# Kernel tuning notes

Measured on AMD Instinct MI355X. Metric: run time of the kernel, lower is better.

Reference implementation:

```python
import jax, jax.numpy as jnp
import numpy as np

D = 512
H = 8
FFN_H = 2048
NEG = -1.0e10


def layer_norm(x, gamma, beta, eps=1e-5):
    mu = jnp.mean(x, axis=-1, keepdims=True)
    var = jnp.var(x, axis=-1, keepdims=True)
    return (x - mu) * jax.lax.rsqrt(var + eps) * gamma + beta


def mha(x_q, x_kv, Wq, Wk, Wv, Wo, valid_lens):
    # x_q: [B,Tq,D], x_kv: [B,Tk,D]; valid_lens: [B,Tq] or [B]
    B, Tq, _ = x_q.shape
    Tk = x_kv.shape[1]
    dh = D // H
    q = (x_q @ Wq.T).reshape(B, Tq, H, dh).transpose(0, 2, 1, 3)  # [B,H,Tq,dh]
    k = (x_kv @ Wk.T).reshape(B, Tk, H, dh).transpose(0, 2, 1, 3)
    v = (x_kv @ Wv.T).reshape(B, Tk, H, dh).transpose(0, 2, 1, 3)
    scores = jnp.einsum('bhqd,bhkd->bhqk', q, k) / jnp.sqrt(jnp.float32(dh))
    pos = jnp.arange(Tk)
    if valid_lens.ndim == 1:  # [B] -> mask [B,1,1,Tk]
        mask = pos[None, None, None, :] < valid_lens[:, None, None, None]
    else:  # [B,Tq] -> mask [B,1,Tq,Tk]
        mask = pos[None, None, None, :] < valid_lens[:, None, :, None]
    scores = jnp.where(mask, scores, NEG)
    attn = jax.nn.softmax(scores, axis=-1)
    out = jnp.einsum('bhqk,bhkd->bhqd', attn, v)  # [B,H,Tq,dh]
    out = out.transpose(0, 2, 1, 3).reshape(B, Tq, D)
    return out @ Wo.T


def setup_inputs() -> dict:
    key = jax.random.key(0)
    ks = jax.random.split(key, 20)
    B, T = 32, 512
    s = 1.0 / np.sqrt(D)
    inp = {
        'X': jax.random.normal(ks[0], (B, T, D), jnp.float32),
        'enc_outputs': jax.random.normal(ks[1], (B, T, D), jnp.float32),
        'dec_valid_lens': jax.random.randint(ks[2], (B, T), 1, T + 1, jnp.int32),
        'enc_valid_lens': jax.random.randint(ks[3], (B,), 1, T + 1, jnp.int32),
    }
    names = ['Wq1', 'Wk1', 'Wv1', 'Wo1', 'Wq2', 'Wk2', 'Wv2', 'Wo2']
    for i, n in enumerate(names):
        inp[n] = jax.random.normal(ks[4 + i], (D, D), jnp.float32) * s
    inp['W1'] = jax.random.normal(ks[12], (FFN_H, D), jnp.float32) * s
    inp['b1'] = jnp.zeros((FFN_H,), jnp.float32)
    inp['W2'] = jax.random.normal(ks[13], (D, FFN_H), jnp.float32) * (1.0 / np.sqrt(FFN_H))
    inp['b2'] = jnp.zeros((D,), jnp.float32)
    for j in (1, 2, 3):
        inp[f'g{j}'] = jnp.ones((D,), jnp.float32)
        inp[f'be{j}'] = jnp.zeros((D,), jnp.float32)
    return inp


def reference(X, enc_outputs, dec_valid_lens, enc_valid_lens,
              Wq1, Wk1, Wv1, Wo1, Wq2, Wk2, Wv2, Wo2,
              W1, b1, W2, b2, g1, be1, g2, be2, g3, be3):
    # Training path: state[2][i] is None -> key_values = X. Dropout in eval mode (identity).
    X2 = mha(X, X, Wq1, Wk1, Wv1, Wo1, dec_valid_lens)            # self-attention
    Y = layer_norm(X + X2, g1, be1)                               # AddNorm1
    Y2 = mha(Y, enc_outputs, Wq2, Wk2, Wv2, Wo2, enc_valid_lens)  # cross-attention
    Z = layer_norm(Y + Y2, g2, be2)                               # AddNorm2
    F = (jax.nn.leaky_relu(Z @ W1.T + b1, 0.01)) @ W2.T + b2      # FFN (LeakyReLU slope 0.01)
    return layer_norm(Z + F, g3, be3)                             # AddNorm3
```

## Files before the change

### kernel.cpp

```cpp
#include <hip/hip_runtime.h>
#include <cstdint>
#include <cstddef>

typedef __bf16 bf16;
typedef __bf16 bf16x8 __attribute__((ext_vector_type(8)));
typedef float  f32x4  __attribute__((ext_vector_type(4)));
typedef unsigned short u16;

#define MD ((size_t)8388608)

__device__ __forceinline__ void async_copy16(const bf16* gp, bf16* lp) {
  __builtin_amdgcn_global_load_lds(
      (__attribute__((address_space(1))) void*)(gp),
      (__attribute__((address_space(3))) void*)(lp), 16, 0, 0);
}

__device__ __forceinline__ int is_f32(const u16* __restrict__ x) {
  const int e = (x[(threadIdx.x & 63) * 2] >> 7) & 0xFF;
  return __ballot(e >= 141) != 0ull;
}

struct ConvSrc { const void* p[20]; };

__global__ __launch_bounds__(256)
void convert_all(ConvSrc s, bf16* __restrict__ ws, const u16* __restrict__ xprobe)
{
  const int n[20] = {8388608, 8388608,
                     262144, 262144, 262144, 262144, 262144, 262144, 262144, 262144,
                     1048576, 2048, 1048576, 512, 512, 512, 512, 512, 512, 512};
  const unsigned int doff[20] = {
      41943040u, 50331648u,
      58720256u, 58982400u, 59244544u, 59506688u,
      59768832u, 60030976u, 60293120u, 60555264u,
      60817408u, 61865984u, 61868032u, 62916608u,
      62917120u, 62917632u, 62918144u, 62918656u, 62919168u, 62919680u};

  const int f32 = is_f32(xprobe);

  int bi = blockIdx.x;
  int idx = 0, b0 = 0;
  for (; idx < 20; ++idx) {
    const int nb = (n[idx] + 2047) >> 11;
    if (bi < b0 + nb) break;
    b0 += nb;
  }
  const int i = ((bi - b0) << 11) + threadIdx.x * 8;
  if (i >= n[idx]) return;
  bf16* dst = ws + doff[idx] + i;
  if (f32) {
    const float* sp = (const float*)s.p[idx] + i;
    f32x4 a = *(const f32x4*)sp;
    f32x4 b = *(const f32x4*)(sp + 4);
    bf16x8 o;
#pragma unroll
    for (int e = 0; e < 4; ++e) { o[e] = (bf16)a[e]; o[4 + e] = (bf16)b[e]; }
    *(bf16x8*)dst = o;
  } else {
    *(bf16x8*)dst = *(const bf16x8*)((const bf16*)s.p[idx] + i);
  }
}

template<int MODE, int TM, int TN>
__global__ __launch_bounds__(256)
void gemm_bt(const bf16* __restrict__ A, const bf16* __restrict__ B,
             const bf16* __restrict__ bias, bf16* __restrict__ C,
             int M, int N, int K)
{
  constexpr int MI = TM / 32;
  constexpr int NJ = TN / 32;
  __shared__ __attribute__((aligned(16))) bf16 As[TM * 64];
  __shared__ __attribute__((aligned(16))) bf16 Bs[TN * 64];

  const int t    = threadIdx.x;
  const int wave = t >> 6;
  const int lane = t & 63;
  const int quad = lane >> 4;
  const int l15  = lane & 15;
  const int wr   = (wave >> 1) * (TM / 2);
  const int wc   = (wave & 1) * (TN / 2);

  const int id    = blockIdx.y * gridDim.x + blockIdx.x;
  const int chunk = (gridDim.x * gridDim.y) >> 3;
  const int lin   = (id & 7) * chunk + (id >> 3);
  const int m0    = (lin / gridDim.x) * TM;
  const int n0    = (lin % gridDim.x) * TN;

  const f32x4 fz = {0.f, 0.f, 0.f, 0.f};
  f32x4 acc[MI][NJ];
#pragma unroll
  for (int i = 0; i < MI; ++i)
#pragma unroll
    for (int j = 0; j < NJ; ++j) acc[i][j] = fz;

  const int nkt = K >> 6;
  for (int kt = 0; kt < nkt; ++kt) {
    const int k0 = kt << 6;
    __syncthreads();
#pragma unroll
    for (int c = 0; c < TM / 32; ++c) {
      const int s   = c * 256 + t;
      const int row = s >> 3;
      const int kg  = ((s & 7) ^ (row & 7)) << 3;
      async_copy16(A + (size_t)(m0 + row) * K + k0 + kg,
                   As + ((c * 256 + wave * 64) << 3));
    }
#pragma unroll
    for (int c = 0; c < TN / 32; ++c) {
      const int s   = c * 256 + t;
      const int row = s >> 3;
      const int kg  = ((s & 7) ^ (row & 7)) << 3;
      async_copy16(B + (size_t)(n0 + row) * K + k0 + kg,
                   Bs + ((c * 256 + wave * 64) << 3));
    }
    __syncthreads();

#pragma unroll
    for (int ks = 0; ks < 2; ++ks) {
      bf16x8 af[MI], bfv[NJ];
#pragma unroll
      for (int i = 0; i < MI; ++i) {
        const int row = wr + i * 16 + l15;
        const int ph  = (ks * 4 + quad) ^ (row & 7);
        af[i] = *(const bf16x8*)(As + row * 64 + ph * 8);
      }
#pragma unroll
      for (int j = 0; j < NJ; ++j) {
        const int row = wc + j * 16 + l15;
        const int ph  = (ks * 4 + quad) ^ (row & 7);
        bfv[j] = *(const bf16x8*)(Bs + row * 64 + ph * 8);
      }
#pragma unroll
      for (int i = 0; i < MI; ++i)
#pragma unroll
        for (int j = 0; j < NJ; ++j)
          acc[i][j] = __builtin_amdgcn_mfma_f32_16x16x32_bf16(af[i], bfv[j],
                                                              acc[i][j], 0, 0, 0);
    }
  }

#pragma unroll
  for (int i = 0; i < MI; ++i) {
    const int m = m0 + wr + i * 16 + quad * 4;
#pragma unroll
    for (int j = 0; j < NJ; ++j) {
      const int n = n0 + wc + j * 16 + l15;
      float bv = 0.f;
      if (MODE >= 1) bv = (float)bias[n];
#pragma unroll
      for (int r = 0; r < 4; ++r) {
        float v = acc[i][j][r];
        if (MODE >= 1) v += bv;
        if (MODE == 1) v = v > 0.f ? v : 0.01f * v;
        C[(size_t)(m + r) * N + n] = (bf16)v;
      }
    }
  }
}

template<int MODE, int BM>
__global__ __launch_bounds__(512, 1)
void gemm4p(const bf16* __restrict__ A, const bf16* __restrict__ B,
            const bf16* __restrict__ bias, bf16* __restrict__ C,
            int M, int N, int K)
{
  constexpr int BN = 256, T = 512, WM = 2, WN = 4;
  constexpr int WR = BM / WM;
  constexpr int MI = WR / 16;
  constexpr int NJ = 4;
  constexpr int MH = MI / 2;
  constexpr int LA = BM * 8 / T;
  constexpr int LB = 4;
  static_assert(LA == 4 || LA == 2, "schedule assumes BM in {256,128}");

  __shared__ __attribute__((aligned(16))) bf16 As[2][BM * 64];
  __shared__ __attribute__((aligned(16))) bf16 Bs[2][BN * 64];

  const int t    = threadIdx.x;
  const int lane = t & 63;
  const int quad = lane >> 4;
  const int l15  = lane & 15;
  const int wave = t >> 6;
  const int wm   = wave >> 2;
  const int wn   = wave & 3;

  const int id    = blockIdx.y * gridDim.x + blockIdx.x;
  const int chunk = (gridDim.x * gridDim.y) >> 3;
  const int lin   = (id & 7) * chunk + (id >> 3);
  const int m0    = (lin / gridDim.x) * BM;
  const int n0    = (lin % gridDim.x) * BN;

  const bf16* Ag = A + (size_t)m0 * K;
  const bf16* Bg = B + (size_t)n0 * K;
  const int wbase = wave << 6;

  auto stA = [&](int kt, int r, int buf) {
    const int s   = r * T + t;
    const int row = s >> 3;
    const int cg  = s & 7;
    async_copy16(Ag + (size_t)row * K + (kt << 6) + ((cg ^ (row & 7)) << 3),
                 &As[buf][(size_t)(r * T + wbase) << 3]);
  };
  auto stB = [&](int kt, int r, int buf) {
    const int s   = r * T + t;
    const int row = s >> 3;
    const int cg  = s & 7;
    async_copy16(Bg + (size_t)row * K + (kt << 6) + ((cg ^ (row & 7)) << 3),
                 &Bs[buf][(size_t)(r * T + wbase) << 3]);
  };
  auto ldfrag = [&](const bf16* base, int row, int ks) -> bf16x8 {
    return *(const bf16x8*)(base + row * 64 + ((((ks << 2) + quad) ^ (row & 7)) << 3));
  };

  const f32x4 fz = {0.f, 0.f, 0.f, 0.f};
  f32x4 acc[MI][NJ];
#pragma unroll
  for (int i = 0; i < MI; ++i)
#pragma unroll
    for (int j = 0; j < NJ; ++j) acc[i][j] = fz;

  const int nkt = K >> 6;

#pragma unroll
  for (int r = 0; r < LA; ++r) stA(0, r, 0);
#pragma unroll
  for (int r = 0; r < LB; ++r) stB(0, r, 0);
  if constexpr (LA == 4) { stA(1, 0, 1); stA(1, 2, 1); }
#pragma unroll
  for (int r = 0; r < LB; ++r) stB(1, r, 1);
  if constexpr (LA == 4) asm volatile("s_waitcnt vmcnt(6)" ::: "memory");
  else                   asm volatile("s_waitcnt vmcnt(4)" ::: "memory");
  __builtin_amdgcn_s_barrier();

  for (int j = 0; j < nkt; ++j) {
    const int cb = j & 1;
    const bf16* a_l = As[cb];
    const bf16* b_l = Bs[cb];
    const int kN = (j + 1 < nkt) ? j + 1 : nkt - 1;
    const int kF = (j + 2 < nkt) ? j + 2 : nkt - 1;

    bf16x8 bfv[NJ];
    bf16x8 af[MH];

#pragma unroll
    for (int nj = 0; nj < NJ; ++nj) bfv[nj] = ldfrag(b_l, wn * 64 + nj * 16 + l15, 0);
#pragma unroll
    for (int mi = 0; mi < MH; ++mi) af[mi] = ldfrag(a_l, wm * WR + mi * 16 + l15, 0);
    if constexpr (LA == 4) { stA(kN, 1, cb ^ 1); stA(kN, 3, cb ^ 1); }
    else                   { stA(kN, 0, cb ^ 1); stA(kN, 1, cb ^ 1); }
    __builtin_amdgcn_s_barrier();
    asm volatile("s_waitcnt lgkmcnt(0)" ::: "memory");
    __builtin_amdgcn_sched_barrier(0);
    __builtin_amdgcn_s_setprio(1);
#pragma unroll
    for (int mi = 0; mi < MH; ++mi)
#pragma unroll
      for (int nj = 0; nj < NJ; ++nj)
        acc[mi][nj] = __builtin_amdgcn_mfma_f32_16x16x32_bf16(af[mi], bfv[nj],
                                                              acc[mi][nj], 0, 0, 0);
    __builtin_amdgcn_s_setprio(0);
    __builtin_amdgcn_s_barrier();

#pragma unroll
    for (int mi = 0; mi < MH; ++mi) af[mi] = ldfrag(a_l, wm * WR + (MH + mi) * 16 + l15, 0);
    __builtin_amdgcn_s_barrier();
    asm volatile("s_waitcnt lgkmcnt(0)" ::: "memory");
    __builtin_amdgcn_sched_barrier(0);
    __builtin_amdgcn_s_setprio(1);
#pragma unroll
    for (int mi = 0; mi < MH; ++mi)
#pragma unroll
      for (int nj = 0; nj < NJ; ++nj)
        acc[MH + mi][nj] = __builtin_amdgcn_mfma_f32_16x16x32_bf16(af[mi], bfv[nj],
                                                                   acc[MH + mi][nj], 0, 0, 0);
    __builtin_amdgcn_s_setprio(0);
    __builtin_amdgcn_s_barrier();

#pragma unroll
    for (int nj = 0; nj < NJ; ++nj) bfv[nj] = ldfrag(b_l, wn * 64 + nj * 16 + l15, 1);
#pragma unroll
    for (int mi = 0; mi < MH; ++mi) af[mi] = ldfrag(a_l, wm * WR + mi * 16 + l15, 1);
    __builtin_amdgcn_s_barrier();
    asm volatile("s_waitcnt lgkmcnt(0)" ::: "memory");
    __builtin_amdgcn_sched_barrier(0);
    __builtin_amdgcn_s_setprio(1);
#pragma unroll
    for (int mi = 0; mi < MH; ++mi)
#pragma unroll
      for (int nj = 0; nj < NJ; ++nj)
        acc[mi][nj] = __builtin_amdgcn_mfma_f32_16x16x32_bf16(af[mi], bfv[nj],
                                                              acc[mi][nj], 0, 0, 0);
    __builtin_amdgcn_s_setprio(0);
    __builtin_amdgcn_s_barrier();

#pragma unroll
    for (int mi = 0; mi < MH; ++mi) af[mi] = ldfrag(a_l, wm * WR + (MH + mi) * 16 + l15, 1);
    if constexpr (LA == 4) { stA(kF, 0, cb); stA(kF, 2, cb); }
#pragma unroll
    for (int r = 0; r < LB; ++r) stB(kF, r, cb);
    __builtin_amdgcn_s_barrier();
    asm volatile("s_waitcnt lgkmcnt(0)" ::: "memory");
    __builtin_amdgcn_sched_barrier(0);
    __builtin_amdgcn_s_setprio(1);
#pragma unroll
    for (int mi = 0; mi < MH; ++mi)
#pragma unroll
      for (int nj = 0; nj < NJ; ++nj)
        acc[MH + mi][nj] = __builtin_amdgcn_mfma_f32_16x16x32_bf16(af[mi], bfv[nj],
                                                                   acc[MH + mi][nj], 0, 0, 0);
    __builtin_amdgcn_s_setprio(0);
    if constexpr (LA == 4) asm volatile("s_waitcnt vmcnt(6)" ::: "memory");
    else                   asm volatile("s_waitcnt vmcnt(4)" ::: "memory");
    __builtin_amdgcn_s_barrier();
  }

  asm volatile("s_waitcnt vmcnt(0)" ::: "memory");

#pragma unroll
  for (int mi = 0; mi < MI; ++mi) {
    const int m = m0 + wm * WR + mi * 16 + quad * 4;
#pragma unroll
    for (int nj = 0; nj < NJ; ++nj) {
      const int n = n0 + wn * 64 + nj * 16 + l15;
      float bv = 0.f;
      if (MODE >= 1) bv = (float)bias[n];
#pragma unroll
      for (int r = 0; r < 4; ++r) {
        float v = acc[mi][nj][r];
        if (MODE >= 1) v += bv;
        if (MODE == 1) v = v > 0.f ? v : 0.01f * v;
        C[(size_t)(m + r) * N + n] = (bf16)v;
      }
    }
  }
}

__global__ __launch_bounds__(256, 4)
void flash_attn(const bf16* __restrict__ Qp, const bf16* __restrict__ Kp,
                const bf16* __restrict__ Vp, bf16* __restrict__ Op,
                const int* __restrict__ vlen, int per_query, int sq, int skv)
{
  __shared__ __attribute__((aligned(16))) bf16 Ks[64][72];
  __shared__ __attribute__((aligned(16))) bf16 VsT[64][72];
  __shared__ __attribute__((aligned(16))) bf16 Ps[4][32][72];
  __shared__ int vlmax_sh;

  const int t    = threadIdx.x;
  const int wave = t >> 6;
  const int lane = t & 63;
  const int quad = lane >> 4;
  const int l15  = lane & 15;
  const int bx   = blockIdx.x;
  const int qt   = bx >> 8;
  const int h    = bx & 7;
  const int b    = (bx >> 3) & 31;
  const int q0   = qt * 128 + wave * 32;

  bf16x8 qfrag[2][2];
#pragma unroll
  for (int mt = 0; mt < 2; ++mt)
#pragma unroll
    for (int ks = 0; ks < 2; ++ks)
      qfrag[mt][ks] = *(const bf16x8*)(Qp +
          (size_t)(b * 512 + q0 + mt * 16 + l15) * sq + h * 64 + ks * 32 + quad * 8);

  int vl_r[2][4];
  int myvl = 1;
#pragma unroll
  for (int mt = 0; mt < 2; ++mt)
#pragma unroll
    for (int r = 0; r < 4; ++r) {
      const int q = q0 + mt * 16 + quad * 4 + r;
      const int v = per_query ? vlen[b * 512 + q] : vlen[b];
      vl_r[mt][r] = v;
      myvl = v > myvl ? v : myvl;
    }

  if (t == 0) vlmax_sh = 1;
  __syncthreads();
#pragma unroll
  for (int off = 1; off < 64; off <<= 1) {
    const int o = __shfl_xor(myvl, off);
    myvl = o > myvl ? o : myvl;
  }
  if (lane == 0) atomicMax(&vlmax_sh, myvl);
  __syncthreads();
  const int ktiles = (vlmax_sh + 63) >> 6;

  const f32x4 fz = {0.f, 0.f, 0.f, 0.f};
  float l_part[2][4] = {{0.f,0.f,0.f,0.f},{0.f,0.f,0.f,0.f}};
  f32x4 o_acc[2][4];
#pragma unroll
  for (int mt = 0; mt < 2; ++mt)
#pragma unroll
    for (int nt = 0; nt < 4; ++nt) o_acc[mt][nt] = fz;

  for (int kt = 0; kt < ktiles; ++kt) {
    const int k0 = kt * 64;
    __syncthreads();
    {
      const int r0 = t >> 3;
      const int c0 = (t & 7) * 8;
      const bf16* g = Kp + (size_t)(b * 512 + k0 + r0) * skv + h * 64 + c0;
      *(bf16x8*)&Ks[r0][c0]      = *(const bf16x8*)g;
      *(bf16x8*)&Ks[r0 + 32][c0] = *(const bf16x8*)(g + (size_t)32 * skv);
    }
    {
      const bf16* g = Vp + (size_t)(b * 512 + k0 + wave * 16) * skv + h * 64 + lane;
      bf16x8 lo, hi;
#pragma unroll
      for (int kk = 0; kk < 8; ++kk) lo[kk] = g[(size_t)kk * skv];
#pragma unroll
      for (int kk = 0; kk < 8; ++kk) hi[kk] = g[(size_t)(kk + 8) * skv];
      *(bf16x8*)&VsT[lane][wave * 16]     = lo;
      *(bf16x8*)&VsT[lane][wave * 16 + 8] = hi;
    }
    __syncthreads();

    f32x4 s[2][4];
#pragma unroll
    for (int mt = 0; mt < 2; ++mt)
#pragma unroll
      for (int nt = 0; nt < 4; ++nt) s[mt][nt] = fz;
#pragma unroll
    for (int ks = 0; ks < 2; ++ks)
#pragma unroll
      for (int nt = 0; nt < 4; ++nt) {
        const bf16x8 bk = *(const bf16x8*)&Ks[nt * 16 + l15][ks * 32 + quad * 8];
        s[0][nt] = __builtin_amdgcn_mfma_f32_16x16x32_bf16(qfrag[0][ks], bk, s[0][nt], 0, 0, 0);
        s[1][nt] = __builtin_amdgcn_mfma_f32_16x16x32_bf16(qfrag[1][ks], bk, s[1][nt], 0, 0, 0);
      }

#pragma unroll
    for (int mt = 0; mt < 2; ++mt)
#pragma unroll
      for (int nt = 0; nt < 4; ++nt) {
        const int k_abs = k0 + nt * 16 + l15;
#pragma unroll
        for (int r = 0; r < 4; ++r) {
          const float p = (k_abs < vl_r[mt][r]) ? __expf(s[mt][nt][r] * 0.125f) : 0.f;
          l_part[mt][r] += p;
          Ps[wave][mt * 16 + quad * 4 + r][nt * 16 + l15] = (bf16)p;
        }
      }

#pragma unroll
    for (int ks = 0; ks < 2; ++ks) {
      const bf16x8 ap0 = *(const bf16x8*)&Ps[wave][l15][ks * 32 + quad * 8];
      const bf16x8 ap1 = *(const bf16x8*)&Ps[wave][16 + l15][ks * 32 + quad * 8];
#pragma unroll
      for (int nt = 0; nt < 4; ++nt) {
        const bf16x8 bv = *(const bf16x8*)&VsT[nt * 16 + l15][ks * 32 + quad * 8];
        o_acc[0][nt] = __builtin_amdgcn_mfma_f32_16x16x32_bf16(ap0, bv, o_acc[0][nt], 0, 0, 0);
        o_acc[1][nt] = __builtin_amdgcn_mfma_f32_16x16x32_bf16(ap1, bv, o_acc[1][nt], 0, 0, 0);
      }
    }
  }

#pragma unroll
  for (int mt = 0; mt < 2; ++mt)
#pragma unroll
    for (int r = 0; r < 4; ++r) {
      float l = l_part[mt][r];
#pragma unroll
      for (int off = 1; off < 16; off <<= 1)
        l += __shfl_xor(l, off);
      const float inv_l = (l > 0.f) ? (1.f / l) : 0.f;
      const int q = q0 + mt * 16 + quad * 4 + r;
#pragma unroll
      for (int nt = 0; nt < 4; ++nt)
        Op[(size_t)(b * 512 + q) * 512 + h * 64 + nt * 16 + l15] =
            (bf16)(o_acc[mt][nt][r] * inv_l);
    }
}

__global__ __launch_bounds__(256)
void add_layernorm(const bf16* X, const bf16* R,
                   const bf16* __restrict__ gamma, const bf16* __restrict__ beta,
                   bf16* Out)
{
  const int t    = threadIdx.x;
  const int wave = t >> 6;
  const int lane = t & 63;
  const size_t row  = (size_t)blockIdx.x * 4 + wave;
  const size_t base = row * 512 + lane * 8;

  bf16x8 xv = *(const bf16x8*)(X + base);
  bf16x8 rv = *(const bf16x8*)(R + base);
  float v[8];
  float sum = 0.f, ss = 0.f;
#pragma unroll
  for (int i = 0; i < 8; ++i) {
    v[i] = (float)xv[i] + (float)rv[i];
    sum += v[i];
    ss  += v[i] * v[i];
  }
#pragma unroll
  for (int off = 1; off < 64; off <<= 1) {
    sum += __shfl_xor(sum, off);
    ss  += __shfl_xor(ss, off);
  }
  const float mean = sum * (1.f / 512.f);
  const float var  = ss * (1.f / 512.f) - mean * mean;
  const float rstd = rsqrtf(var + 1e-5f);

  bf16x8 gv = *(const bf16x8*)(gamma + lane * 8);
  bf16x8 bv = *(const bf16x8*)(beta + lane * 8);
  bf16x8 ov;
#pragma unroll
  for (int i = 0; i < 8; ++i)
    ov[i] = (bf16)(((v[i] - mean) * rstd) * (float)gv[i] + (float)bv[i]);
  *(bf16x8*)(Out + base) = ov;
}

__global__ __launch_bounds__(256)
void add_layernorm_out(const bf16* X, const bf16* R,
                       const bf16* __restrict__ gamma, const bf16* __restrict__ beta,
                       void* Out, const u16* __restrict__ xprobe)
{
  const int t    = threadIdx.x;
  const int wave = t >> 6;
  const int lane = t & 63;
  const size_t row  = (size_t)blockIdx.x * 4 + wave;
  const size_t base = row * 512 + lane * 8;

  const int f32 = is_f32(xprobe);

  bf16x8 xv = *(const bf16x8*)(X + base);
  bf16x8 rv = *(const bf16x8*)(R + base);
  float v[8];
  float sum = 0.f, ss = 0.f;
#pragma unroll
  for (int i = 0; i < 8; ++i) {
    v[i] = (float)xv[i] + (float)rv[i];
    sum += v[i];
    ss  += v[i] * v[i];
  }
#pragma unroll
  for (int off = 1; off < 64; off <<= 1) {
    sum += __shfl_xor(sum, off);
    ss  += __shfl_xor(ss, off);
  }
  const float mean = sum * (1.f / 512.f);
  const float var  = ss * (1.f / 512.f) - mean * mean;
  const float rstd = rsqrtf(var + 1e-5f);

  bf16x8 gv = *(const bf16x8*)(gamma + lane * 8);
  bf16x8 bv = *(const bf16x8*)(beta + lane * 8);
  float o[8];
#pragma unroll
  for (int i = 0; i < 8; ++i)
    o[i] = ((v[i] - mean) * rstd) * (float)gv[i] + (float)bv[i];

  if (f32) {
    float* op = (float*)Out + base;
    f32x4 o0 = {o[0], o[1], o[2], o[3]};
    f32x4 o1 = {o[4], o[5], o[6], o[7]};
    *(f32x4*)op       = o0;
    *(f32x4*)(op + 4) = o1;
  } else {
    bf16x8 ov;
#pragma unroll
    for (int i = 0; i < 8; ++i) ov[i] = (bf16)o[i];
    *(bf16x8*)((bf16*)Out + base) = ov;
  }
}

extern "C" void kernel_launch(void* const* d_in, const int* in_sizes, int n_in,
                              void* d_out, int out_size, void* d_ws, size_t ws_size,
                              hipStream_t stream)
{
  (void)in_sizes; (void)n_in; (void)out_size; (void)ws_size;

  const int* dvl = (const int*)d_in[2];
  const int* evl = (const int*)d_in[3];
  const u16* xprobe = (const u16*)d_in[0];

  bf16* ws = (bf16*)d_ws;
  bf16* S0 = ws;
  bf16* S1 = ws + 1 * MD;
  bf16* S3 = ws + 3 * MD;
  bf16* S4 = ws + 4 * MD;
  bf16* Xb = ws + 5 * MD;
  bf16* Eb = ws + 6 * MD;
  bf16* W  = ws + 7 * MD;
  const bf16 *Wq1 = W,
             *Wo1 = W + 786432,   *Wq2 = W + 1048576, *Wk2 = W + 1310720,
             *Wo2 = W + 1835008,
             *W1  = W + 2097152,  *b1  = W + 3145728,
             *W2  = W + 3147776,  *b2  = W + 4196352,
             *g1  = W + 4196864,  *be1 = W + 4197376,
             *g2  = W + 4197888,  *be2 = W + 4198400,
             *g3  = W + 4198912,  *be3 = W + 4199424;

  ConvSrc cs;
  cs.p[0] = d_in[0];  cs.p[1] = d_in[1];
  for (int k = 0; k < 12; ++k) cs.p[2 + k] = d_in[4 + k];
  for (int k = 0; k < 6; ++k)  cs.p[14 + k] = d_in[16 + k];
  convert_all<<<dim3(10248), dim3(256), 0, stream>>>(cs, ws, xprobe);

  dim3 blk256(256);
  dim3 blk512(512);
  dim3 gP(4, 128);

  gemm4p<0,256><<<dim3(6, 64), blk512, 0, stream>>>(Xb, Wq1, nullptr, S0, 16384, 1536, 512);
  flash_attn<<<dim3(1024), blk256, 0, stream>>>(S0, S0 + 512, S0 + 1024, S3, dvl, 1, 1536, 1536);
  gemm_bt<0,128,128><<<gP, blk256, 0, stream>>>(S3, Wo1, nullptr, S1, 16384, 512, 512);
  add_layernorm<<<dim3(4096), blk256, 0, stream>>>(Xb, S1, g1, be1, S4);

  gemm_bt<0,128,128><<<gP, blk256, 0, stream>>>(S4, Wq2, nullptr, S0, 16384, 512, 512);
  gemm4p<0,256><<<dim3(4, 64), blk512, 0, stream>>>(Eb, Wk2, nullptr, S1, 16384, 1024, 512);
  flash_attn<<<dim3(1024), blk256, 0, stream>>>(S0, S1, S1 + 512, S3, evl, 0, 512, 1024);
  gemm_bt<0,128,128><<<gP, blk256, 0, stream>>>(S3, Wo2, nullptr, S1, 16384, 512, 512);
  add_layernorm<<<dim3(4096), blk256, 0, stream>>>(S4, S1, g2, be2, S4);

  gemm4p<1,256><<<dim3(8, 64), blk512, 0, stream>>>(S4, W1, b1, S0, 16384, 2048, 512);
  gemm4p<2,128><<<dim3(2, 128), blk512, 0, stream>>>(S0, W2, b2, Xb, 16384, 512, 2048);
  add_layernorm_out<<<dim3(4096), blk256, 0, stream>>>(S4, Xb, g3, be3, d_out, xprobe);
}
```

Before: 469.3 us.

## Merge independent projection GEMMs into one launch and use pipelined GEMM for 512-wide projections

The self-attention QKV projection and the cross-attention KV projection are independent, so they now run in a single 640-block launch that dispatches on block index. This fills more of the device at once and removes one launch boundary. The 512-output projections (Wo1, Wq2, Wo2) move from the simple single-buffered gemm_bt to the double-buffered 512-thread gemm4p with BM=128. That variant gives only 256 blocks per launch, so occupancy on those smaller GEMMs may drop. Workspace buffers are reassigned to avoid aliasing between the now-reordered stages.

```diff
diff --git a/kernel.cpp b/kernel.cpp
--- a/kernel.cpp
+++ b/kernel.cpp
@@ -60,108 +60,11 @@
   }
 }
 
-template<int MODE, int TM, int TN>
-__global__ __launch_bounds__(256)
-void gemm_bt(const bf16* __restrict__ A, const bf16* __restrict__ B,
-             const bf16* __restrict__ bias, bf16* __restrict__ C,
-             int M, int N, int K)
-{
-  constexpr int MI = TM / 32;
-  constexpr int NJ = TN / 32;
-  __shared__ __attribute__((aligned(16))) bf16 As[TM * 64];
-  __shared__ __attribute__((aligned(16))) bf16 Bs[TN * 64];
-
-  const int t    = threadIdx.x;
-  const int wave = t >> 6;
-  const int lane = t & 63;
-  const int quad = lane >> 4;
-  const int l15  = lane & 15;
-  const int wr   = (wave >> 1) * (TM / 2);
-  const int wc   = (wave & 1) * (TN / 2);
-
-  const int id    = blockIdx.y * gridDim.x + blockIdx.x;
-  const int chunk = (gridDim.x * gridDim.y) >> 3;
-  const int lin   = (id & 7) * chunk + (id >> 3);
-  const int m0    = (lin / gridDim.x) * TM;
-  const int n0    = (lin % gridDim.x) * TN;
-
-  const f32x4 fz = {0.f, 0.f, 0.f, 0.f};
-  f32x4 acc[MI][NJ];
-#pragma unroll
-  for (int i = 0; i < MI; ++i)
-#pragma unroll
-    for (int j = 0; j < NJ; ++j) acc[i][j] = fz;
-
-  const int nkt = K >> 6;
-  for (int kt = 0; kt < nkt; ++kt) {
-    const int k0 = kt << 6;
-    __syncthreads();
-#pragma unroll
-    for (int c = 0; c < TM / 32; ++c) {
-      const int s   = c * 256 + t;
-      const int row = s >> 3;
-      const int kg  = ((s & 7) ^ (row & 7)) << 3;
-      async_copy16(A + (size_t)(m0 + row) * K + k0 + kg,
-                   As + ((c * 256 + wave * 64) << 3));
-    }
-#pragma unroll
-    for (int c = 0; c < TN / 32; ++c) {
-      const int s   = c * 256 + t;
-      const int row = s >> 3;
-      const int kg  = ((s & 7) ^ (row & 7)) << 3;
-      async_copy16(B + (size_t)(n0 + row) * K + k0 + kg,
-                   Bs + ((c * 256 + wave * 64) << 3));
-    }
-    __syncthreads();
-
-#pragma unroll
-    for (int ks = 0; ks < 2; ++ks) {
-      bf16x8 af[MI], bfv[NJ];
-#pragma unroll
-      for (int i = 0; i < MI; ++i) {
-        const int row = wr + i * 16 + l15;
-        const int ph  = (ks * 4 + quad) ^ (row & 7);
-        af[i] = *(const bf16x8*)(As + row * 64 + ph * 8);
-      }
-#pragma unroll
-      for (int j = 0; j < NJ; ++j) {
-        const int row = wc + j * 16 + l15;
-        const int ph  = (ks * 4 + quad) ^ (row & 7);
-        bfv[j] = *(const bf16x8*)(Bs + row * 64 + ph * 8);
-      }
-#pragma unroll
-      for (int i = 0; i < MI; ++i)
-#pragma unroll
-        for (int j = 0; j < NJ; ++j)
-          acc[i][j] = __builtin_amdgcn_mfma_f32_16x16x32_bf16(af[i], bfv[j],
-                                                              acc[i][j], 0, 0, 0);
-    }
-  }
-
-#pragma unroll
-  for (int i = 0; i < MI; ++i) {
-    const int m = m0 + wr + i * 16 + quad * 4;
-#pragma unroll
-    for (int j = 0; j < NJ; ++j) {
-      const int n = n0 + wc + j * 16 + l15;
-      float bv = 0.f;
-      if (MODE >= 1) bv = (float)bias[n];
-#pragma unroll
-      for (int r = 0; r < 4; ++r) {
-        float v = acc[i][j][r];
-        if (MODE >= 1) v += bv;
-        if (MODE == 1) v = v > 0.f ? v : 0.01f * v;
-        C[(size_t)(m + r) * N + n] = (bf16)v;
-      }
-    }
-  }
-}
-
 template<int MODE, int BM>
-__global__ __launch_bounds__(512, 1)
-void gemm4p(const bf16* __restrict__ A, const bf16* __restrict__ B,
-            const bf16* __restrict__ bias, bf16* __restrict__ C,
-            int M, int N, int K)
+__device__ __forceinline__ void gemm4p_body(
+    const bf16* __restrict__ A, const bf16* __restrict__ B,
+    const bf16* __restrict__ bias, bf16* __restrict__ C,
+    int N, int K, int gx, int bid, int nblk, bf16* AsP, bf16* BsP)
 {
   constexpr int BN = 256, T = 512, WM = 2, WN = 4;
   constexpr int WR = BM / WM;
@@ -172,9 +75,6 @@
   constexpr int LB = 4;
   static_assert(LA == 4 || LA == 2, "schedule assumes BM in {256,128}");
 
-  __shared__ __attribute__((aligned(16))) bf16 As[2][BM * 64];
-  __shared__ __attribute__((aligned(16))) bf16 Bs[2][BN * 64];
-
   const int t    = threadIdx.x;
   const int lane = t & 63;
   const int quad = lane >> 4;
@@ -183,11 +83,10 @@
   const int wm   = wave >> 2;
   const int wn   = wave & 3;
 
-  const int id    = blockIdx.y * gridDim.x + blockIdx.x;
-  const int chunk = (gridDim.x * gridDim.y) >> 3;
-  const int lin   = (id & 7) * chunk + (id >> 3);
-  const int m0    = (lin / gridDim.x) * BM;
-  const int n0    = (lin % gridDim.x) * BN;
+  const int chunk = nblk >> 3;
+  const int lin   = (bid & 7) * chunk + (bid >> 3);
+  const int m0    = (lin / gx) * BM;
+  const int n0    = (lin % gx) * BN;
 
   const bf16* Ag = A + (size_t)m0 * K;
   const bf16* Bg = B + (size_t)n0 * K;
@@ -198,14 +97,14 @@
     const int row = s >> 3;
     const int cg  = s & 7;
     async_copy16(Ag + (size_t)row * K + (kt << 6) + ((cg ^ (row & 7)) << 3),
-                 &As[buf][(size_t)(r * T + wbase) << 3]);
+                 AsP + buf * (BM * 64) + ((size_t)(r * T + wbase) << 3));
   };
   auto stB = [&](int kt, int r, int buf) {
     const int s   = r * T + t;
     const int row = s >> 3;
     const int cg  = s & 7;
     async_copy16(Bg + (size_t)row * K + (kt << 6) + ((cg ^ (row & 7)) << 3),
-                 &Bs[buf][(size_t)(r * T + wbase) << 3]);
+                 BsP + buf * (BN * 64) + ((size_t)(r * T + wbase) << 3));
   };
   auto ldfrag = [&](const bf16* base, int row, int ks) -> bf16x8 {
     return *(const bf16x8*)(base + row * 64 + ((((ks << 2) + quad) ^ (row & 7)) << 3));
@@ -233,8 +132,8 @@
 
   for (int j = 0; j < nkt; ++j) {
     const int cb = j & 1;
-    const bf16* a_l = As[cb];
-    const bf16* b_l = Bs[cb];
+    const bf16* a_l = AsP + cb * (BM * 64);
+    const bf16* b_l = BsP + cb * (BN * 64);
     const int kN = (j + 1 < nkt) ? j + 1 : nkt - 1;
     const int kF = (j + 2 < nkt) ? j + 2 : nkt - 1;
 
@@ -332,6 +231,32 @@
       }
     }
   }
+}
+
+template<int MODE, int BM>
+__global__ __launch_bounds__(512, 1)
+void gemm4p(const bf16* __restrict__ A, const bf16* __restrict__ B,
+            const bf16* __restrict__ bias, bf16* __restrict__ C,
+            int N, int K, int gx)
+{
+  __shared__ __attribute__((aligned(16))) bf16 As[2 * BM * 64];
+  __shared__ __attribute__((aligned(16))) bf16 Bs[2 * 256 * 64];
+  gemm4p_body<MODE, BM>(A, B, bias, C, N, K, gx, blockIdx.x, gridDim.x, As, Bs);
+}
+
+__global__ __launch_bounds__(512, 1)
+void gemm4p_dual(const bf16* __restrict__ A0, const bf16* __restrict__ B0,
+                 bf16* __restrict__ C0,
+                 const bf16* __restrict__ A1, const bf16* __restrict__ B1,
+                 bf16* __restrict__ C1)
+{
+  __shared__ __attribute__((aligned(16))) bf16 As[2 * 256 * 64];
+  __shared__ __attribute__((aligned(16))) bf16 Bs[2 * 256 * 64];
+  const int bid = blockIdx.x;
+  if (bid < 384)
+    gemm4p_body<0, 256>(A0, B0, nullptr, C0, 1536, 512, 6, bid, 384, As, Bs);
+  else
+    gemm4p_body<0, 256>(A1, B1, nullptr, C1, 1024, 512, 4, bid - 384, 256, As, Bs);
 }
 
 __global__ __launch_bounds__(256, 4)
@@ -578,6 +503,7 @@
   bf16* ws = (bf16*)d_ws;
   bf16* S0 = ws;
   bf16* S1 = ws + 1 * MD;
+  bf16* S2 = ws + 2 * MD;
   bf16* S3 = ws + 3 * MD;
   bf16* S4 = ws + 4 * MD;
   bf16* Xb = ws + 5 * MD;
@@ -600,20 +526,19 @@
 
   dim3 blk256(256);
   dim3 blk512(512);
-  dim3 gP(4, 128);
-
-  gemm4p<0,256><<<dim3(6, 64), blk512, 0, stream>>>(Xb, Wq1, nullptr, S0, 16384, 1536, 512);
-  flash_attn<<<dim3(1024), blk256, 0, stream>>>(S0, S0 + 512, S0 + 1024, S3, dvl, 1, 1536, 1536);
-  gemm_bt<0,128,128><<<gP, blk256, 0, stream>>>(S3, Wo1, nullptr, S1, 16384, 512, 512);
-  add_layernorm<<<dim3(4096), blk256, 0, stream>>>(Xb, S1, g1, be1, S4);
-
-  gemm_bt<0,128,128><<<gP, blk256, 0, stream>>>(S4, Wq2, nullptr, S0, 16384, 512, 512);
-  gemm4p<0,256><<<dim3(4, 64), blk512, 0, stream>>>(Eb, Wk2, nullptr, S1, 16384, 1024, 512);
-  flash_attn<<<dim3(1024), blk256, 0, stream>>>(S0, S1, S1 + 512, S3, evl, 0, 512, 1024);
-  gemm_bt<0,128,128><<<gP, blk256, 0, stream>>>(S3, Wo2, nullptr, S1, 16384, 512, 512);
-  add_layernorm<<<dim3(4096), blk256, 0, stream>>>(S4, S1, g2, be2, S4);
-
-  gemm4p<1,256><<<dim3(8, 64), blk512, 0, stream>>>(S4, W1, b1, S0, 16384, 2048, 512);
-  gemm4p<2,128><<<dim3(2, 128), blk512, 0, stream>>>(S0, W2, b2, Xb, 16384, 512, 2048);
+
+  gemm4p_dual<<<dim3(640), blk512, 0, stream>>>(Xb, Wq1, S0, Eb, Wk2, S3);
+
+  flash_attn<<<dim3(1024), blk256, 0, stream>>>(S0, S0 + 512, S0 + 1024, Eb, dvl, 1, 1536, 1536);
+  gemm4p<0,128><<<dim3(256), blk512, 0, stream>>>(Eb, Wo1, nullptr, S0, 512, 512, 2);
+  add_layernorm<<<dim3(4096), blk256, 0, stream>>>(Xb, S0, g1, be1, S1);
+
+  gemm4p<0,128><<<dim3(256), blk512, 0, stream>>>(S1, Wq2, nullptr, S2, 512, 512, 2);
+  flash_attn<<<dim3(1024), blk256, 0, stream>>>(S2, S3, S3 + 512, S0, evl, 0, 512, 1024);
+  gemm4p<0,128><<<dim3(256), blk512, 0, stream>>>(S0, Wo2, nullptr, S2, 512, 512, 2);
+  add_layernorm<<<dim3(4096), blk256, 0, stream>>>(S1, S2, g2, be2, S4);
+
+  gemm4p<1,256><<<dim3(512), blk512, 0, stream>>>(S4, W1, b1, S0, 2048, 512, 8);
+  gemm4p<2,128><<<dim3(256), blk512, 0, stream>>>(S0, W2, b2, Xb, 512, 2048, 2);
   add_layernorm_out<<<dim3(4096), blk256, 0, stream>>>(S4, Xb, g3, be3, d_out, xprobe);
 }
```

Result: no change. 465.1 us (-0.9%).
